# Kernel tuning notes

Hardware: AMD Instinct MI355X
Metric: run time of the kernel (lower is better)

## Reference

```python
import jax, jax.numpy as jnp
import numpy as np

T, H, I, E, K = 2048, 1024, 4096, 8, 2
SOFTCAP = 30.0


def setup_inputs() -> dict:
    key = jax.random.key(0)
    k1, k2, k3, k4, k5 = jax.random.split(key, 5)
    scale = 0.02
    x = jax.random.normal(k1, (T, H), dtype=jnp.float32)
    gate_w = jax.random.normal(k2, (E, H), dtype=jnp.float32) * scale  # router weight [E, H]
    w1g = jax.random.normal(k3, (E, I, H), dtype=jnp.float32) * scale  # gate proj
    w1u = jax.random.normal(k4, (E, I, H), dtype=jnp.float32) * scale  # up proj
    w2 = jax.random.normal(k5, (E, H, I), dtype=jnp.float32) * scale   # down proj
    return {"x": x, "gate_w": gate_w, "w1g": w1g, "w1u": w1u, "w2": w2}


def reference(x, gate_w, w1g, w1u, w2):
    # --- Router: fp32 logits, tanh softcap, softmax, top-k (no renormalize) ---
    logits = x.astype(jnp.float32) @ gate_w.T            # [T, E]
    capped = SOFTCAP * jnp.tanh(logits / SOFTCAP)
    probs = jax.nn.softmax(capped, axis=-1)              # [T, E]
    topk_w, topk_ids = jax.lax.top_k(probs, K)           # [T, K], [T, K]
    topk_w = topk_w.astype(x.dtype)

    # --- Experts: gated GLU FFN with erf-GELU, weighted combine ---
    out = jnp.zeros_like(x)
    for e in range(E):  # E is a small structural constant
        we = jnp.sum(topk_w * (topk_ids == e), axis=-1)  # [T] combine weight (0 if not routed)
        g = jax.nn.gelu(x @ w1g[e].T, approximate=False)  # [T, I]
        h = g * (x @ w1u[e].T)                            # [T, I]
        out = out + (h @ w2[e].T) * we[:, None]           # [T, H]
    return out
```

## Files before the change

### kernel.cpp

```cpp
#include <hip/hip_runtime.h>
#include <hip/hip_bf16.h>
#include <stdint.h>

#define T_TOK 2048
#define H_DIM 1024
#define I_DIM 4096
#define E_NUM 8

#define GBM 256
#define BM 128
#define BN 64
#define BK 64
#define KS 2

typedef unsigned short u16;
typedef __bf16 bf16_t;
typedef bf16_t bf16x8 __attribute__((ext_vector_type(8)));
typedef float f32x4 __attribute__((ext_vector_type(4)));

__device__ __forceinline__ u16 f2bf(float f) {
  union { float f; unsigned u; } a; a.f = f;
  unsigned r = a.u + 0x7FFFu + ((a.u >> 16) & 1u);
  return (u16)(r >> 16);
}

__device__ __forceinline__ void gload_lds16(const void* g, void* l) {
  __builtin_amdgcn_global_load_lds(
      (const __attribute__((address_space(1))) void*)g,
      (__attribute__((address_space(3))) void*)l, 16, 0, 0);
}

__device__ __forceinline__ float gelu_fast(float g) {
  float y = g * (0.7978845608f + 0.0356774081f * g * g);
  return g / (1.0f + __expf(-2.0f * y));
}

__device__ __forceinline__ uint4 pack8(float4 f0, float4 f1) {
  union { uint4 u; u16 s[8]; } p;
  p.s[0] = f2bf(f0.x); p.s[1] = f2bf(f0.y); p.s[2] = f2bf(f0.z); p.s[3] = f2bf(f0.w);
  p.s[4] = f2bf(f1.x); p.s[5] = f2bf(f1.y); p.s[6] = f2bf(f1.z); p.s[7] = f2bf(f1.w);
  return p.u;
}

__global__ __launch_bounds__(256) void k_prep(const float* __restrict__ x,
                                              float* __restrict__ out,
                                              u16* __restrict__ xb,
                                              int* __restrict__ counts) {
  int i = blockIdx.x * 256 + threadIdx.x;
  if (i < E_NUM) counts[i] = 0;
  float4 v = reinterpret_cast<const float4*>(x)[i];
  ushort4 b;
  b.x = f2bf(v.x); b.y = f2bf(v.y); b.z = f2bf(v.z); b.w = f2bf(v.w);
  reinterpret_cast<ushort4*>(xb)[i] = b;
  reinterpret_cast<float4*>(out)[i] = make_float4(0.f, 0.f, 0.f, 0.f);
}

__global__ __launch_bounds__(256) void k_router(const float* __restrict__ x,
                                                const float* __restrict__ gw,
                                                int* __restrict__ counts,
                                                int* __restrict__ ids,
                                                float* __restrict__ wts) {
  int gtid = blockIdx.x * 256 + threadIdx.x;
  int t = gtid >> 6;
  int lane = threadIdx.x & 63;
  if (t >= T_TOK) return;
  const float* xr = x + (size_t)t * H_DIM;
  float4 xv[4];
#pragma unroll
  for (int j = 0; j < 4; ++j) xv[j] = reinterpret_cast<const float4*>(xr)[lane + 64 * j];
  float logit[E_NUM];
#pragma unroll
  for (int e = 0; e < E_NUM; ++e) {
    const float4* gr = reinterpret_cast<const float4*>(gw + (size_t)e * H_DIM);
    float s = 0.f;
#pragma unroll
    for (int j = 0; j < 4; ++j) {
      float4 g = gr[lane + 64 * j];
      s += xv[j].x * g.x + xv[j].y * g.y + xv[j].z * g.z + xv[j].w * g.w;
    }
#pragma unroll
    for (int off = 32; off; off >>= 1) s += __shfl_xor(s, off);
    logit[e] = s;
  }
  if (lane == 0) {
    float cap[E_NUM], mx = -1e30f;
#pragma unroll
    for (int e = 0; e < E_NUM; ++e) {
      cap[e] = 30.f * tanhf(logit[e] * (1.f / 30.f));
      mx = fmaxf(mx, cap[e]);
    }
    float p[E_NUM], sum = 0.f;
#pragma unroll
    for (int e = 0; e < E_NUM; ++e) { p[e] = expf(cap[e] - mx); sum += p[e]; }
    int i1 = 0; float p1 = p[0];
#pragma unroll
    for (int e = 1; e < E_NUM; ++e) if (p[e] > p1) { p1 = p[e]; i1 = e; }
    int i2 = -1; float p2 = -1.f;
#pragma unroll
    for (int e = 0; e < E_NUM; ++e) if (e != i1 && p[e] > p2) { p2 = p[e]; i2 = e; }
    float inv = 1.f / sum;
    int s1 = atomicAdd(&counts[i1], 1);
    ids[i1 * T_TOK + s1] = t; wts[i1 * T_TOK + s1] = p1 * inv;
    int s2 = atomicAdd(&counts[i2], 1);
    ids[i2 * T_TOK + s2] = t; wts[i2 * T_TOK + s2] = p2 * inv;
  }
}

__global__ void k_offs(const int* __restrict__ counts, int* __restrict__ offs) {
  if (threadIdx.x == 0) {
    int a = 0;
    for (int e = 0; e < E_NUM; ++e) { offs[e] = a; a += counts[e]; }
  }
}

__global__ __launch_bounds__(512) void k_gateup4(
    const u16* __restrict__ xb, const float* __restrict__ w1g, const float* __restrict__ w1u,
    const float* __restrict__ w2, u16* __restrict__ w2b,
    const int* __restrict__ counts, const int* __restrict__ offs, const int* __restrict__ ids,
    u16* __restrict__ h) {
  if (blockIdx.z == E_NUM) {
    int bid = blockIdx.y * (I_DIM / BN) + blockIdx.x;
    const int N4 = E_NUM * H_DIM * I_DIM / 4;
    for (int i = bid * 512 + threadIdx.x; i < N4; i += 512 * 512) {
      float4 v = reinterpret_cast<const float4*>(w2)[i];
      ushort4 b;
      b.x = f2bf(v.x); b.y = f2bf(v.y); b.z = f2bf(v.z); b.w = f2bf(v.w);
      reinterpret_cast<ushort4*>(w2b)[i] = b;
    }
    return;
  }
  const int e = blockIdx.z, mt = blockIdx.y, nt = blockIdx.x;
  const int cnt = counts[e];
  if (mt * GBM >= cnt) return;
  __shared__ u16 As[2 * GBM * BK];
  __shared__ u16 Bg[BN * BK];
  __shared__ u16 Bu[BN * BK];
  const int tid = threadIdx.x, lane = tid & 63, wid = tid >> 6;
  const int wr = (wid >> 1) * 64, wc = (wid & 1) * 32;
  const int lr = lane & 15, lk = lane >> 4;
  const int i0 = nt * BN;
  const int lrow = lane >> 3;
  const int lgs = (lane & 7) ^ (lrow & 7);
  const int sw = lr & 7;

  const u16* asrc[4];
#pragma unroll
  for (int i = 0; i < 4; ++i) {
    int rg = mt * GBM + wid * 32 + i * 8 + lrow;
    if (rg >= cnt) rg = cnt - 1;
    asrc[i] = xb + (size_t)ids[e * T_TOK + rg] * H_DIM + lgs * 8;
  }
  u16* aldsb = As + (wid * 32) * BK;

  const int br = tid >> 3, bc = tid & 7;
  const float* gsrc = w1g + (size_t)(e * I_DIM + i0 + br) * H_DIM + bc * 8;
  const float* usrc = w1u + (size_t)(e * I_DIM + i0 + br) * H_DIM + bc * 8;
  const int wgo = br * BK + (((bc) ^ (br & 7)) << 3);
  float4 RG0, RG1, RU0, RU1;
  auto LOADB = [&](int ko) {
    RG0 = *reinterpret_cast<const float4*>(gsrc + ko);
    RG1 = *reinterpret_cast<const float4*>(gsrc + ko + 4);
    RU0 = *reinterpret_cast<const float4*>(usrc + ko);
    RU1 = *reinterpret_cast<const float4*>(usrc + ko + 4);
  };
  auto WRITEB = [&]() {
    *reinterpret_cast<uint4*>(&Bg[wgo]) = pack8(RG0, RG1);
    *reinterpret_cast<uint4*>(&Bu[wgo]) = pack8(RU0, RU1);
  };
  auto STAGE_A = [&](int buf, int ko) {
#pragma unroll
    for (int i = 0; i < 4; ++i)
      gload_lds16(asrc[i] + ko, aldsb + buf * GBM * BK + i * 8 * BK);
  };

  f32x4 accg[4][2], accu[4][2];
#pragma unroll
  for (int mi = 0; mi < 4; ++mi)
#pragma unroll
    for (int ni = 0; ni < 2; ++ni) { accg[mi][ni] = (f32x4)0.f; accu[mi][ni] = (f32x4)0.f; }

  LOADB(0);
  STAGE_A(0, 0);
  WRITEB();
  __syncthreads();

  const int NT = H_DIM / BK;
  for (int kt = 0; kt < NT; ++kt) {
    const int cur = kt & 1;
    if (kt + 1 < NT) {
      LOADB((kt + 1) * BK);
      STAGE_A(cur ^ 1, (kt + 1) * BK);
    }
#pragma unroll
    for (int kk = 0; kk < 2; ++kk) {
      const int colg = kk * 4 + lk;
      const int gsw = (colg ^ sw) << 3;
      bf16x8 a[4], bg[2], bu[2];
#pragma unroll
      for (int mi = 0; mi < 4; ++mi)
        a[mi] = *reinterpret_cast<const bf16x8*>(&As[cur * GBM * BK + (wr + mi * 16 + lr) * BK + gsw]);
#pragma unroll
      for (int ni = 0; ni < 2; ++ni) {
        bg[ni] = *reinterpret_cast<const bf16x8*>(&Bg[(wc + ni * 16 + lr) * BK + gsw]);
        bu[ni] = *reinterpret_cast<const bf16x8*>(&Bu[(wc + ni * 16 + lr) * BK + gsw]);
      }
#pragma unroll
      for (int mi = 0; mi < 4; ++mi)
#pragma unroll
        for (int ni = 0; ni < 2; ++ni) {
          accg[mi][ni] = __builtin_amdgcn_mfma_f32_16x16x32_bf16(a[mi], bg[ni], accg[mi][ni], 0, 0, 0);
          accu[mi][ni] = __builtin_amdgcn_mfma_f32_16x16x32_bf16(a[mi], bu[ni], accu[mi][ni], 0, 0, 0);
        }
    }
    if (kt + 1 < NT) {
      __syncthreads();
      WRITEB();
      __syncthreads();
    }
  }

  const int hbase = offs[e];
#pragma unroll
  for (int mi = 0; mi < 4; ++mi)
#pragma unroll
    for (int rr = 0; rr < 4; ++rr) {
      int grow = mt * GBM + wr + mi * 16 + lk * 4 + rr;
      if (grow < cnt) {
        size_t hrow = (size_t)(hbase + grow) * I_DIM;
#pragma unroll
        for (int ni = 0; ni < 2; ++ni) {
          int col = i0 + wc + ni * 16 + lr;
          h[hrow + col] = f2bf(gelu_fast(accg[mi][ni][rr]) * accu[mi][ni][rr]);
        }
      }
    }
}

__global__ __launch_bounds__(256) void k_down2(
    const u16* __restrict__ h, const u16* __restrict__ w2b,
    const int* __restrict__ counts, const int* __restrict__ offs, const int* __restrict__ ids,
    const float* __restrict__ wts, float* __restrict__ out) {
  const int e = blockIdx.z, mt = blockIdx.y;
  const int nt = blockIdx.x & 15, ks = blockIdx.x >> 4;
  const int cnt = counts[e];
  if (mt * BM >= cnt) return;
  __shared__ u16 As[2 * BM * BK];
  __shared__ u16 Bs[2 * BN * BK];
  const int tid = threadIdx.x, lane = tid & 63, wid = tid >> 6;
  const int wr = (wid >> 1) * 64, wc = (wid & 1) * 32;
  const int lr = lane & 15, lk = lane >> 4;
  const int n0 = nt * BN;
  const int hbase = offs[e];
  const int lrow = lane >> 3;
  const int lgs = (lane & 7) ^ (lrow & 7);
  const int sw = lr & 7;

  const u16* asrc[4];
#pragma unroll
  for (int i = 0; i < 4; ++i) {
    int rg = mt * BM + wid * 32 + i * 8 + lrow;
    if (rg >= cnt) rg = cnt - 1;
    asrc[i] = h + (size_t)(hbase + rg) * I_DIM + lgs * 8;
  }
  const u16* bsrc[2];
#pragma unroll
  for (int i = 0; i < 2; ++i)
    bsrc[i] = w2b + (size_t)(e * H_DIM + n0 + wid * 16 + i * 8 + lrow) * I_DIM + lgs * 8;
  u16* aldsb = As + (wid * 32) * BK;
  u16* bldsb = Bs + (wid * 16) * BK;

  auto STAGE = [&](int buf, int ko) {
#pragma unroll
    for (int i = 0; i < 4; ++i) gload_lds16(asrc[i] + ko, aldsb + buf * BM * BK + i * 8 * BK);
#pragma unroll
    for (int i = 0; i < 2; ++i) gload_lds16(bsrc[i] + ko, bldsb + buf * BN * BK + i * 8 * BK);
  };

  f32x4 acc[4][2];
#pragma unroll
  for (int mi = 0; mi < 4; ++mi)
#pragma unroll
    for (int ni = 0; ni < 2; ++ni) acc[mi][ni] = (f32x4)0.f;

  const int KT = I_DIM / BK / KS;
  const int kbase = ks * KT * BK;
  STAGE(0, kbase);
  __syncthreads();

  for (int kt = 0; kt < KT; ++kt) {
    const int cur = kt & 1;
    if (kt + 1 < KT) STAGE(cur ^ 1, kbase + (kt + 1) * BK);
#pragma unroll
    for (int kk = 0; kk < 2; ++kk) {
      const int colg = kk * 4 + lk;
      const int gsw = (colg ^ sw) << 3;
      bf16x8 a[4], b[2];
#pragma unroll
      for (int mi = 0; mi < 4; ++mi)
        a[mi] = *reinterpret_cast<const bf16x8*>(&As[cur * BM * BK + (wr + mi * 16 + lr) * BK + gsw]);
#pragma unroll
      for (int ni = 0; ni < 2; ++ni)
        b[ni] = *reinterpret_cast<const bf16x8*>(&Bs[cur * BN * BK + (wc + ni * 16 + lr) * BK + gsw]);
#pragma unroll
      for (int mi = 0; mi < 4; ++mi)
#pragma unroll
        for (int ni = 0; ni < 2; ++ni)
          acc[mi][ni] = __builtin_amdgcn_mfma_f32_16x16x32_bf16(a[mi], b[ni], acc[mi][ni], 0, 0, 0);
    }
    __syncthreads();
  }

#pragma unroll
  for (int mi = 0; mi < 4; ++mi)
#pragma unroll
    for (int rr = 0; rr < 4; ++rr) {
      int grow = mt * BM + wr + mi * 16 + lk * 4 + rr;
      if (grow < cnt) {
        int tok = ids[e * T_TOK + grow];
        float w = wts[e * T_TOK + grow];
#pragma unroll
        for (int ni = 0; ni < 2; ++ni) {
          int col = n0 + wc + ni * 16 + lr;
          atomicAdd(&out[(size_t)tok * H_DIM + col], w * acc[mi][ni][rr]);
        }
      }
    }
}

extern "C" void kernel_launch(void* const* d_in, const int* in_sizes, int n_in,
                              void* d_out, int out_size, void* d_ws, size_t ws_size,
                              hipStream_t stream) {
  const float* x   = (const float*)d_in[0];
  const float* gw  = (const float*)d_in[1];
  const float* w1g = (const float*)d_in[2];
  const float* w1u = (const float*)d_in[3];
  const float* w2  = (const float*)d_in[4];
  float* out = (float*)d_out;
  char* ws = (char*)d_ws;

  const size_t MB = 1u << 20;
  const size_t OFF_XB  = 0;
  const size_t OFF_H   = 4 * MB;
  const size_t OFF_W2B = OFF_H + 32 * MB;
  const size_t OFF_IDS = OFF_W2B + 64 * MB;
  const size_t OFF_WTS = OFF_IDS + (64u << 10);
  const size_t OFF_CNT = OFF_WTS + (64u << 10);

  u16* xb     = (u16*)(ws + OFF_XB);
  u16* h      = (u16*)(ws + OFF_H);
  u16* w2b    = (u16*)(ws + OFF_W2B);
  int* ids    = (int*)(ws + OFF_IDS);
  float* wts  = (float*)(ws + OFF_WTS);
  int* counts = (int*)(ws + OFF_CNT);
  int* offs   = counts + 8;

  k_prep<<<2048, 256, 0, stream>>>(x, out, xb, counts);
  k_router<<<512, 256, 0, stream>>>(x, gw, counts, ids, wts);
  k_offs<<<1, 64, 0, stream>>>(counts, offs);
  k_gateup4<<<dim3(I_DIM / BN, T_TOK / GBM, E_NUM + 1), 512, 0, stream>>>(
      xb, w1g, w1u, w2, w2b, counts, offs, ids, h);
  k_down2<<<dim3((H_DIM / BN) * KS, T_TOK / BM, E_NUM), 256, 0, stream>>>(
      h, w2b, counts, offs, ids, wts, out);
}
```

Baseline: 335.9 us.

## Convert down-proj weights to bf16 on the fly instead of a pre-pass

Removes the separate full fp32-to-bf16 conversion of w2 into a workspace buffer, which ran as extra blocks of the gate/up kernel. The down-projection kernel now loads fp32 w2 tiles into registers, packs them to bf16, and writes them to a single-buffered LDS tile, with an extra barrier pair each k-step. This avoids writing and re-reading 64MB of bf16 weights, but each w2 tile is now read as fp32 by every M-tile block, which doubles B-operand bytes, and the B operand loses double buffering.

```diff
diff --git a/kernel.cpp b/kernel.cpp
--- a/kernel.cpp
+++ b/kernel.cpp
@@ -115,20 +115,8 @@
 
 __global__ __launch_bounds__(512) void k_gateup4(
     const u16* __restrict__ xb, const float* __restrict__ w1g, const float* __restrict__ w1u,
-    const float* __restrict__ w2, u16* __restrict__ w2b,
     const int* __restrict__ counts, const int* __restrict__ offs, const int* __restrict__ ids,
     u16* __restrict__ h) {
-  if (blockIdx.z == E_NUM) {
-    int bid = blockIdx.y * (I_DIM / BN) + blockIdx.x;
-    const int N4 = E_NUM * H_DIM * I_DIM / 4;
-    for (int i = bid * 512 + threadIdx.x; i < N4; i += 512 * 512) {
-      float4 v = reinterpret_cast<const float4*>(w2)[i];
-      ushort4 b;
-      b.x = f2bf(v.x); b.y = f2bf(v.y); b.z = f2bf(v.z); b.w = f2bf(v.w);
-      reinterpret_cast<ushort4*>(w2b)[i] = b;
-    }
-    return;
-  }
   const int e = blockIdx.z, mt = blockIdx.y, nt = blockIdx.x;
   const int cnt = counts[e];
   if (mt * GBM >= cnt) return;
@@ -236,8 +224,8 @@
     }
 }
 
-__global__ __launch_bounds__(256) void k_down2(
-    const u16* __restrict__ h, const u16* __restrict__ w2b,
+__global__ __launch_bounds__(256) void k_down9(
+    const u16* __restrict__ h, const float* __restrict__ w2,
     const int* __restrict__ counts, const int* __restrict__ offs, const int* __restrict__ ids,
     const float* __restrict__ wts, float* __restrict__ out) {
   const int e = blockIdx.z, mt = blockIdx.y;
@@ -245,7 +233,7 @@
   const int cnt = counts[e];
   if (mt * BM >= cnt) return;
   __shared__ u16 As[2 * BM * BK];
-  __shared__ u16 Bs[2 * BN * BK];
+  __shared__ u16 Bs[BN * BK];
   const int tid = threadIdx.x, lane = tid & 63, wid = tid >> 6;
   const int wr = (wid >> 1) * 64, wc = (wid & 1) * 32;
   const int lr = lane & 15, lk = lane >> 4;
@@ -262,18 +250,27 @@
     if (rg >= cnt) rg = cnt - 1;
     asrc[i] = h + (size_t)(hbase + rg) * I_DIM + lgs * 8;
   }
-  const u16* bsrc[2];
-#pragma unroll
-  for (int i = 0; i < 2; ++i)
-    bsrc[i] = w2b + (size_t)(e * H_DIM + n0 + wid * 16 + i * 8 + lrow) * I_DIM + lgs * 8;
   u16* aldsb = As + (wid * 32) * BK;
-  u16* bldsb = Bs + (wid * 16) * BK;
-
-  auto STAGE = [&](int buf, int ko) {
-#pragma unroll
-    for (int i = 0; i < 4; ++i) gload_lds16(asrc[i] + ko, aldsb + buf * BM * BK + i * 8 * BK);
-#pragma unroll
-    for (int i = 0; i < 2; ++i) gload_lds16(bsrc[i] + ko, bldsb + buf * BN * BK + i * 8 * BK);
+
+  const int brw = tid >> 2, bc4 = tid & 3;
+  const float* bsrc = w2 + (size_t)(e * H_DIM + n0 + brw) * I_DIM + bc4 * 16;
+  const int wg0 = brw * BK + (((bc4 * 2) ^ (brw & 7)) << 3);
+  const int wg1 = brw * BK + (((bc4 * 2 + 1) ^ (brw & 7)) << 3);
+  float4 RB0, RB1, RB2, RB3;
+  auto LOADB = [&](int ko) {
+    RB0 = *reinterpret_cast<const float4*>(bsrc + ko);
+    RB1 = *reinterpret_cast<const float4*>(bsrc + ko + 4);
+    RB2 = *reinterpret_cast<const float4*>(bsrc + ko + 8);
+    RB3 = *reinterpret_cast<const float4*>(bsrc + ko + 12);
+  };
+  auto WRITEB = [&]() {
+    *reinterpret_cast<uint4*>(&Bs[wg0]) = pack8(RB0, RB1);
+    *reinterpret_cast<uint4*>(&Bs[wg1]) = pack8(RB2, RB3);
+  };
+  auto STAGE_A = [&](int buf, int ko) {
+#pragma unroll
+    for (int i = 0; i < 4; ++i)
+      gload_lds16(asrc[i] + ko, aldsb + buf * BM * BK + i * 8 * BK);
   };
 
   f32x4 acc[4][2];
@@ -284,12 +281,17 @@
 
   const int KT = I_DIM / BK / KS;
   const int kbase = ks * KT * BK;
-  STAGE(0, kbase);
+  LOADB(kbase);
+  STAGE_A(0, kbase);
+  WRITEB();
   __syncthreads();
 
   for (int kt = 0; kt < KT; ++kt) {
     const int cur = kt & 1;
-    if (kt + 1 < KT) STAGE(cur ^ 1, kbase + (kt + 1) * BK);
+    if (kt + 1 < KT) {
+      LOADB(kbase + (kt + 1) * BK);
+      STAGE_A(cur ^ 1, kbase + (kt + 1) * BK);
+    }
 #pragma unroll
     for (int kk = 0; kk < 2; ++kk) {
       const int colg = kk * 4 + lk;
@@ -300,14 +302,18 @@
         a[mi] = *reinterpret_cast<const bf16x8*>(&As[cur * BM * BK + (wr + mi * 16 + lr) * BK + gsw]);
 #pragma unroll
       for (int ni = 0; ni < 2; ++ni)
-        b[ni] = *reinterpret_cast<const bf16x8*>(&Bs[cur * BN * BK + (wc + ni * 16 + lr) * BK + gsw]);
+        b[ni] = *reinterpret_cast<const bf16x8*>(&Bs[(wc + ni * 16 + lr) * BK + gsw]);
 #pragma unroll
       for (int mi = 0; mi < 4; ++mi)
 #pragma unroll
         for (int ni = 0; ni < 2; ++ni)
           acc[mi][ni] = __builtin_amdgcn_mfma_f32_16x16x32_bf16(a[mi], b[ni], acc[mi][ni], 0, 0, 0);
     }
-    __syncthreads();
+    if (kt + 1 < KT) {
+      __syncthreads();
+      WRITEB();
+      __syncthreads();
+    }
   }
 
 #pragma unroll
@@ -341,14 +347,12 @@
   const size_t MB = 1u << 20;
   const size_t OFF_XB  = 0;
   const size_t OFF_H   = 4 * MB;
-  const size_t OFF_W2B = OFF_H + 32 * MB;
-  const size_t OFF_IDS = OFF_W2B + 64 * MB;
+  const size_t OFF_IDS = OFF_H + 32 * MB;
   const size_t OFF_WTS = OFF_IDS + (64u << 10);
   const size_t OFF_CNT = OFF_WTS + (64u << 10);
 
   u16* xb     = (u16*)(ws + OFF_XB);
   u16* h      = (u16*)(ws + OFF_H);
-  u16* w2b    = (u16*)(ws + OFF_W2B);
   int* ids    = (int*)(ws + OFF_IDS);
   float* wts  = (float*)(ws + OFF_WTS);
   int* counts = (int*)(ws + OFF_CNT);
@@ -357,8 +361,8 @@
   k_prep<<<2048, 256, 0, stream>>>(x, out, xb, counts);
   k_router<<<512, 256, 0, stream>>>(x, gw, counts, ids, wts);
   k_offs<<<1, 64, 0, stream>>>(counts, offs);
-  k_gateup4<<<dim3(I_DIM / BN, T_TOK / GBM, E_NUM + 1), 512, 0, stream>>>(
-      xb, w1g, w1u, w2, w2b, counts, offs, ids, h);
-  k_down2<<<dim3((H_DIM / BN) * KS, T_TOK / BM, E_NUM), 256, 0, stream>>>(
-      h, w2b, counts, offs, ids, wts, out);
-}
+  k_gateup4<<<dim3(I_DIM / BN, T_TOK / GBM, E_NUM), 512, 0, stream>>>(
+      xb, w1g, w1u, counts, offs, ids, h);
+  k_down9<<<dim3((H_DIM / BN) * KS, T_TOK / BM, E_NUM), 256, 0, stream>>>(
+      h, w2, counts, offs, ids, wts, out);
+}
```

Result: faster. 303.0 us (-9.8%).
